# Performance work log

Hardware: AMD Instinct MI355X
Metric: run time of the kernel (lower is better)

Reference implementation:

```python
import jax, jax.numpy as jnp
import numpy as np

# config constants (match init_kwargs)
T, B = 32, 32
H, W_IN, C_IN = 128, 128, 2
FH, FW = 32, 32
CF, CP = 64, 32
OUT = 128
PATCH = 8
TOPK_R = 4
KWTA = 16
SPARSITY = 0.5
BETA = 0.9
VTH = 1.0
EVT = 0.5
PH, PW = H // PATCH, W_IN // PATCH  # 16,16


def _topk_mask(x, k):
    # mask of entries >= k-th largest along last axis
    k = min(k, x.shape[-1])
    if k <= 0:
        return jnp.zeros_like(x)
    top_vals = jax.lax.top_k(x, k)[0]
    thresh = top_vals[..., k - 1:k]
    return (x >= thresh).astype(x.dtype)


def _block_sparse_mask(w, sparsity, block=4):
    h, wk, cin, cout = w.shape
    bh, bw = h // block, wk // block
    if bh == 0 or bw == 0:
        # 3x3 kernel with block=4 degenerates to a dense (all-ones) mask
        return jnp.ones((h, wk, 1, 1), dtype=w.dtype)
    core = w[:bh * block, :bw * block, :, :]
    blocks = core.reshape(bh, block, bw, block, cin, cout)
    scores = jnp.mean(jnp.abs(blocks), axis=(1, 3, 4, 5)).reshape(-1)
    keep = max(1, int(scores.shape[0] * (1.0 - sparsity)))
    gate = _topk_mask(scores[None, :], keep).reshape(bh, bw)
    gate = jnp.repeat(jnp.repeat(gate, block, axis=0), block, axis=1)
    mask = jnp.ones((h, wk), dtype=w.dtype).at[:bh * block, :bw * block].set(gate)
    return mask[:, :, None, None]


def _conv(x, w):
    return jax.lax.conv_general_dilated(
        x, w, (1, 1), 'SAME', dimension_numbers=('NHWC', 'HWIO', 'NHWC'))


@jax.custom_vjp
def _spike(v):
    return (v > 0).astype(v.dtype)

def _spike_fwd(v):
    return _spike(v), v

def _spike_bwd(v, g):
    # superspike surrogate gradient (k=25)
    return (g / (1.0 + 25.0 * jnp.abs(v)) ** 2,)

_spike.defvjp(_spike_fwd, _spike_bwd)


def setup_inputs() -> dict:
    key = jax.random.key(0)
    ks = jax.random.split(key, 8)
    def vs_uniform(k, shape):
        # VarianceScaling(1.0, fan_avg, uniform)
        fan_in = shape[0] * shape[1] * shape[2] if len(shape) == 4 else shape[0]
        fan_out = shape[0] * shape[1] * shape[3] if len(shape) == 4 else shape[1]
        limit = float(np.sqrt(3.0 / ((fan_in + fan_out) / 2.0)))
        return jax.random.uniform(k, shape, jnp.float32, -limit, limit)
    return {
        'x_seq': jax.random.normal(ks[0], (T, B, H, W_IN, C_IN), jnp.float32),
        'w_fovea': vs_uniform(ks[1], (3, 3, C_IN, CF)),
        'w_periph': vs_uniform(ks[2], (3, 3, C_IN, CP)),
        'head_w': vs_uniform(ks[3], (CF + CP, OUT)),
        'head_b': jnp.zeros((OUT,), jnp.float32),
        'route_w': vs_uniform(ks[4], (PH * PW, OUT)),
        'route_b': jnp.zeros((OUT,), jnp.float32),
    }


def reference(x_seq, w_fovea, w_periph, head_w, head_b, route_w, route_b):
    # block-sparse masks are constant across time: apply once
    w_f = w_fovea * _block_sparse_mask(w_fovea, SPARSITY)
    w_p = w_periph * _block_sparse_mask(w_periph, SPARSITY)

    def step(carry, x_t):
        vf, vp = carry
        event_mask = (jnp.abs(x_t) > EVT).astype(x_t.dtype)
        xs = x_t * event_mask
        # region activation router: mean |x| per patch
        patches = xs.reshape(B, PH, PATCH, PW, PATCH, C_IN)
        scores = jnp.mean(jnp.abs(patches), axis=(2, 4, 5)).reshape(B, PH * PW)
        region_gate = _topk_mask(scores, TOPK_R)
        # foveal crop around the best patch
        best = jnp.argmax(scores, axis=-1)
        cy = best // PW * PATCH + PATCH // 2
        cx = best % PW * PATCH + PATCH // 2
        y0 = jnp.clip(cy - FH // 2, 0, H - FH)
        x0 = jnp.clip(cx - FW // 2, 0, W_IN - FW)
        fovea = jax.vmap(
            lambda img, y, x: jax.lax.dynamic_slice(img, (y, x, 0), (FH, FW, C_IN))
        )(xs, y0, x0)
        # fovea conv + k-WTA channel gate
        ff = _conv(fovea, w_f)
        sal = jnp.mean(jnp.abs(ff), axis=(1, 2))            # (B, CF)
        channel_gate = _topk_mask(sal, KWTA)
        ff = ff * channel_gate[:, None, None, :]
        # periphery: half-res linear resize + conv
        periph = jax.image.resize(xs, (B, H // 2, W_IN // 2, C_IN), method='linear')
        pf = _conv(periph, w_p)
        # LIF updates (beta decay, threshold, soft reset)
        vf = BETA * vf + ff
        sf = _spike(vf - VTH)
        vf = vf - sf * VTH
        vp = BETA * vp + pf
        sp = _spike(vp - VTH)
        vp = vp - sp * VTH
        fused = jnp.concatenate([jnp.mean(sf, axis=(1, 2)), jnp.mean(sp, axis=(1, 2))], axis=-1)
        logits_t = fused @ head_w + head_b + scores @ route_w + route_b
        sr_t = jnp.stack([jnp.mean(sf), jnp.mean(sp)])
        active_ratio = jnp.mean(event_mask)
        route_stats = jnp.mean(region_gate, axis=0)
        chan_stats = jnp.mean(channel_gate, axis=0)
        return (vf, vp), (logits_t, sr_t, active_ratio, route_stats, chan_stats)

    vf0 = jnp.zeros((B, FH, FW, CF), x_seq.dtype)
    vp0 = jnp.zeros((B, H // 2, W_IN // 2, CP), x_seq.dtype)
    _, (logits_seq, sr_seq, active_seq, route_seq, chan_seq) = jax.lax.scan(
        step, (vf0, vp0), x_seq)
    out = jnp.mean(logits_seq, axis=0)  # readout='mean'
    return (out, logits_seq, jnp.mean(sr_seq, axis=0), jnp.mean(active_seq),
            jnp.mean(route_seq, axis=0), jnp.mean(chan_seq, axis=0))
```

## Files before the change

kernel.cpp:

```cpp
#include <hip/hip_runtime.h>

#define T_ 32
#define B_ 32
#define H_ 128
#define W_ 128
#define C_ 2
#define NP_ 256
#define CF_ 64
#define CP_ 32
#define OUT_ 128

#define PROW 136
#define PTB  8976
#define WTB  2312

#define OFF_LOGITS 4096
#define OFF_SR     135168
#define OFF_ACTIVE 135170
#define OFF_ROUTE  135171
#define OFF_CHAN   135427

#define CNT_N 323

typedef float f2 __attribute__((ext_vector_type(2)));

__device__ __forceinline__ float f4c(const float4& v, int i) {
  switch (i & 3) { case 0: return v.x; case 1: return v.y; case 2: return v.z; default: return v.w; }
}

__global__ void __launch_bounds__(256) k_pre(const float* __restrict__ x,
    const float* __restrict__ wf,
    float* __restrict__ scores_g, float* __restrict__ P, float* __restrict__ Wfbuf,
    float* __restrict__ chan_gate, unsigned* __restrict__ cnts) {
  const int tb = blockIdx.x, tid = threadIdx.x;
  __shared__ __align__(16) float xt[34*256];
  __shared__ float sm[NP_];
  __shared__ float salred[512];
  __shared__ float salv[64];
  __shared__ unsigned wsum[4];
  __shared__ float wred[4];
  __shared__ int widx[4];
  __shared__ int2 syx;
  const float* img = x + (size_t)tb*32768;
  unsigned cnt = 0;
  for (int chunk = 0; chunk < 4; ++chunk) {
    const int r0 = chunk*16;
    __syncthreads();
    for (int i4 = tid; i4 < 34*64; i4 += 256) {
      const int rr = i4 >> 6, off4 = i4 & 63;
      const int xr = 2*r0 - 1 + rr;
      float4 vv = make_float4(0.f, 0.f, 0.f, 0.f);
      if (xr >= 0 && xr < H_) {
        vv = *reinterpret_cast<const float4*>(img + (size_t)xr*256 + off4*4);
        if (rr >= 1 && rr <= 32) {
          cnt += (fabsf(vv.x) > 0.5f) + (fabsf(vv.y) > 0.5f)
               + (fabsf(vv.z) > 0.5f) + (fabsf(vv.w) > 0.5f);
        }
        vv.x = (fabsf(vv.x) > 0.5f) ? vv.x : 0.f;
        vv.y = (fabsf(vv.y) > 0.5f) ? vv.y : 0.f;
        vv.z = (fabsf(vv.z) > 0.5f) ? vv.z : 0.f;
        vv.w = (fabsf(vv.w) > 0.5f) ? vv.w : 0.f;
      }
      *reinterpret_cast<float4*>(&xt[i4*4]) = vv;
    }
    __syncthreads();
    {
      const int patch = tid >> 2, q = tid & 3;
      const int prl = patch >> 4, pc = patch & 15;
      const int row = 1 + prl*8 + q*2;
      float s = 0.f;
#pragma unroll
      for (int r2 = 0; r2 < 2; ++r2)
#pragma unroll
        for (int j = 0; j < 4; ++j) {
          const float4 vv = *reinterpret_cast<const float4*>(&xt[(row + r2)*256 + pc*16 + j*4]);
          s += fabsf(vv.x) + fabsf(vv.y) + fabsf(vv.z) + fabsf(vv.w);
        }
      s += __shfl_down(s, 1);
      s += __shfl_down(s, 2);
      if (q == 0) {
        const float sv = s * (1.f/128.f);
        sm[chunk*64 + patch] = sv;
        scores_g[tb*NP_ + chunk*64 + patch] = sv;
      }
    }
    float* Pt = P + (size_t)tb * PTB;
    if (tid < 128) {
      const int r = tid >> 3, rem = tid & 7;
      const int px4 = rem >> 1, ci = rem & 1;
      const int px = (px4 < 2) ? (px4 - 2) : (62 + px4);
      Pt[(r0 + r + 1)*PROW + (px + 2)*2 + ci] = 0.f;
    }
    if (chunk == 0 && tid < PROW) Pt[tid] = 0.f;
    if (chunk == 3 && tid < PROW) Pt[65*PROW + tid] = 0.f;
#pragma unroll
    for (int k = 0; k < 4; ++k) {
      const int idx = k*256 + tid;
      const int col = idx & 63, row16 = idx >> 6;
      const int pr = r0 + row16;
      float wy0=0.125f, wy1=0.375f, wy2=0.375f, wy3=0.125f;
      if (pr == 0)       { wy0=0.f;     wy1=3.f/7.f; wy2=3.f/7.f; wy3=1.f/7.f; }
      else if (pr == 63) { wy0=1.f/7.f; wy1=3.f/7.f; wy2=3.f/7.f; wy3=0.f; }
      float wx0=0.125f, wx1=0.375f, wx2=0.375f, wx3=0.125f;
      if (col == 0)       { wx0=0.f;     wx1=3.f/7.f; wx2=3.f/7.f; wx3=1.f/7.f; }
      else if (col == 63) { wx0=1.f/7.f; wx1=3.f/7.f; wx2=3.f/7.f; wx3=0.f; }
      const int lr = 2*row16;
      const int cc0 = 2*col - 1;
      f2 val = (f2)0.f;
#pragma unroll
      for (int j = 0; j < 4; ++j) {
        const float wyj = (j==0)?wy0:(j==1)?wy1:(j==2)?wy2:wy3;
        f2 h = (f2)0.f;
#pragma unroll
        for (int i = 0; i < 4; ++i) {
          const float wxi = (i==0)?wx0:(i==1)?wx1:(i==2)?wx2:wx3;
          int cc = cc0 + i; cc = cc < 0 ? 0 : (cc > W_-1 ? W_-1 : cc);
          const f2 xv = *reinterpret_cast<const f2*>(&xt[(lr + j)*256 + cc*2]);
          h += wxi * xv;
        }
        val += wyj * h;
      }
      *reinterpret_cast<f2*>(&Pt[(pr + 1)*PROW + (col + 2)*2]) = val;
    }
  }
  unsigned c64 = cnt;
#pragma unroll
  for (int off = 32; off > 0; off >>= 1) c64 += __shfl_down(c64, off);
  if ((tid & 63) == 0) wsum[tid >> 6] = c64;
  __syncthreads();
  if (tid == 0) atomicAdd(&cnts[0], wsum[0] + wsum[1] + wsum[2] + wsum[3]);
  {
    const float sv_ = sm[tid];
    const int wv = tid >> 6, ln = tid & 63;
    bool masked = false;
    float v4 = 0.f;
    for (int r = 0; r < 4; ++r) {
      float cur = masked ? -1e30f : sv_;
      float m = cur;
#pragma unroll
      for (int off = 32; off > 0; off >>= 1) m = fmaxf(m, __shfl_xor(m, off));
      if (ln == 0) wred[wv] = m;
      __syncthreads();
      const float bm = fmaxf(fmaxf(wred[0], wred[1]), fmaxf(wred[2], wred[3]));
      const unsigned long long eq = __ballot(cur == bm);
      if (ln == 0) widx[wv] = eq ? (wv*64 + (int)(__ffsll((long long)eq) - 1)) : 1024;
      __syncthreads();
      const int first = min(min(widx[0], widx[1]), min(widx[2], widx[3]));
      if (tid == first) {
        masked = true;
        if (r == 0) {
          const int cy = (tid >> 4)*8 + 4, cx = (tid & 15)*8 + 4;
          int y0 = cy - 16; y0 = y0 < 0 ? 0 : (y0 > 96 ? 96 : y0);
          int x0 = cx - 16; x0 = x0 < 0 ? 0 : (x0 > 96 ? 96 : x0);
          syx = make_int2(y0, x0);
        }
      }
      if (r == 3) v4 = bm;
      __syncthreads();
    }
    if (sv_ >= v4) atomicAdd(&cnts[1 + tid], 1u);
  }
  float* tile = xt;
  for (int i = tid; i < 34*68; i += 256) tile[i] = 0.f;
  __syncthreads();
  const int2 yx = syx;
  {
    const int row = tid >> 3, seg = tid & 7;
    const float* src = img + (size_t)(yx.x + row)*256 + (yx.y + seg*4)*2;
    float4 a = *reinterpret_cast<const float4*>(src);
    float4 b4 = *reinterpret_cast<const float4*>(src + 4);
    a.x  = (fabsf(a.x)  > 0.5f) ? a.x  : 0.f;
    a.y  = (fabsf(a.y)  > 0.5f) ? a.y  : 0.f;
    a.z  = (fabsf(a.z)  > 0.5f) ? a.z  : 0.f;
    a.w  = (fabsf(a.w)  > 0.5f) ? a.w  : 0.f;
    b4.x = (fabsf(b4.x) > 0.5f) ? b4.x : 0.f;
    b4.y = (fabsf(b4.y) > 0.5f) ? b4.y : 0.f;
    b4.z = (fabsf(b4.z) > 0.5f) ? b4.z : 0.f;
    b4.w = (fabsf(b4.w) > 0.5f) ? b4.w : 0.f;
    float* dst = &tile[(row + 1)*68 + (seg*4 + 1)*2];
    *reinterpret_cast<float2*>(dst)     = make_float2(a.x, a.y);
    *reinterpret_cast<float2*>(dst + 2) = make_float2(a.z, a.w);
    *reinterpret_cast<float2*>(dst + 4) = make_float2(b4.x, b4.y);
    *reinterpret_cast<float2*>(dst + 6) = make_float2(b4.z, b4.w);
  }
  __syncthreads();
  {
    float* dst = Wfbuf + (size_t)tb*WTB;
    for (int i = tid; i < WTB/4; i += 256)
      *reinterpret_cast<float4*>(dst + i*4) = *reinterpret_cast<const float4*>(&tile[i*4]);
  }
  const int cp2 = tid & 31, xg = tid >> 5;
  const int c0 = cp2*2;
  f2 wxr[9], wyr[9];
#pragma unroll
  for (int j = 0; j < 9; ++j) {
    wxr[j] = *reinterpret_cast<const f2*>(&wf[(2*j)*CF_ + c0]);
    wyr[j] = *reinterpret_cast<const f2*>(&wf[(2*j + 1)*CF_ + c0]);
  }
  const float* tbase = &tile[xg*8];
  float4 wb[3][3];
#pragma unroll
  for (int m = 0; m < 3; ++m) {
    wb[0][m] = *reinterpret_cast<const float4*>(tbase + m*4);
    wb[1][m] = *reinterpret_cast<const float4*>(tbase + 68 + m*4);
  }
  f2 sal = (f2)0.f;
#pragma unroll
  for (int yy = 0; yy < 32; ++yy) {
#pragma unroll
    for (int m = 0; m < 3; ++m)
      wb[(yy+2)%3][m] = *reinterpret_cast<const float4*>(tbase + (yy+2)*68 + m*4);
#pragma unroll
    for (int k = 0; k < 4; ++k) {
      f2 acc = (f2)0.f;
#pragma unroll
      for (int dy = 0; dy < 3; ++dy) {
#pragma unroll
        for (int dx = 0; dx < 3; ++dx) {
          const int r = k + dx;
          const float4 f = wb[(yy+dy)%3][r >> 1];
          acc += f4c(f, (r&1)*2)     * wxr[dy*3+dx]
               + f4c(f, (r&1)*2 + 1) * wyr[dy*3+dx];
        }
      }
      sal.x += fabsf(acc.x);
      sal.y += fabsf(acc.y);
    }
  }
  salred[xg*64 + c0]     = sal.x;
  salred[xg*64 + c0 + 1] = sal.y;
  __syncthreads();
  if (tid < 64) {
    float s = 0.f;
#pragma unroll
    for (int g = 0; g < 8; ++g) s += salred[g*64 + tid];
    salv[tid] = s * (1.f/1024.f);
  }
  __syncthreads();
  if (tid < 64) {
    const float sv = salv[tid];
    int cg = 0;
    for (int q = 0; q < 64; ++q) cg += (salv[q] > sv) ? 1 : 0;
    const float gate = (cg < 16) ? 1.f : 0.f;
    chan_gate[tb*CF_ + tid] = gate;
    if (gate > 0.f) atomicAdd(&cnts[257 + tid], 1u);
  }
}

__global__ void __launch_bounds__(256, 2) k_mem(const float* __restrict__ Wfbuf,
    const float* __restrict__ P, const float* __restrict__ wf, const float* __restrict__ wp,
    const float* __restrict__ chan_gate,
    unsigned* __restrict__ fov_part, unsigned* __restrict__ per_part) {
  __shared__ __align__(16) float lds[2*1360];
  const int tid = threadIdx.x;
  const int w = tid >> 6, l = tid & 63;
  int zp;
  asm volatile("v_mov_b32 %0, 0" : "=v"(zp));
  if (blockIdx.x < 1024) {
    const int blk = blockIdx.x;
    const int b = blk >> 5, rem = blk & 31, cp = rem >> 1, half = rem & 1;
    const int ch0 = cp*4;
    const int brow = w*4 + (l >> 4);
    const int po = (l & 15)*4;
    f2 w01[18], w23[18];
#pragma unroll
    for (int k = 0; k < 18; ++k) {
      w01[k] = *reinterpret_cast<const f2*>(&wf[k*CF_ + ch0 + zp]);
      w23[k] = *reinterpret_cast<const f2*>(&wf[k*CF_ + ch0 + zp + 2]);
    }
    const float* gsrc = Wfbuf + (size_t)b*WTB + half*16*68;
    const float* gp = chan_gate + b*CF_ + ch0 + zp;
    const unsigned ob01 = (unsigned)((b*32 + cp*2)*8 + half*4 + w);
    f2 va01 = (f2)0.f, vb01 = (f2)0.f, va23 = (f2)0.f, vb23 = (f2)0.f;
    float4 r0, r1;
    r0 = *reinterpret_cast<const float4*>(gsrc + tid*4);
    if (tid < 50) r1 = *reinterpret_cast<const float4*>(gsrc + (tid + 256)*4);
    *reinterpret_cast<float4*>(&lds[tid*4]) = r0;
    if (tid < 50) *reinterpret_cast<float4*>(&lds[(tid + 256)*4]) = r1;
    int cur = 0;
    for (int t = 0; t < T_; ++t) {
      __syncthreads();
      if (t + 1 < T_) {
        const float* gn = gsrc + (size_t)(t + 1)*(B_*WTB);
        r0 = *reinterpret_cast<const float4*>(gn + tid*4);
        if (tid < 50) r1 = *reinterpret_cast<const float4*>(gn + (tid + 256)*4);
      }
      __builtin_amdgcn_sched_barrier(0);
      const f2 g01 = *reinterpret_cast<const f2*>(gp + (size_t)t*B_*CF_);
      const f2 g23 = *reinterpret_cast<const f2*>(gp + (size_t)t*B_*CF_ + 2);
      const float* Lb = &lds[cur*1360];
      f2 aa01 = (f2)0.f, ab01 = (f2)0.f, aa23 = (f2)0.f, ab23 = (f2)0.f;
#pragma unroll
      for (int dy = 0; dy < 3; ++dy) {
        const float4 fa = *reinterpret_cast<const float4*>(Lb + (brow + dy)*68 + po);
        const float4 fb = *reinterpret_cast<const float4*>(Lb + (brow + dy)*68 + po + 4);
        {
          const f2 w0 = w01[dy*6], w0y = w01[dy*6+1], w1 = w01[dy*6+2],
                   w1y = w01[dy*6+3], w2 = w01[dy*6+4], w2y = w01[dy*6+5];
          aa01 += fa.x*w0 + fa.y*w0y + fa.z*w1 + fa.w*w1y + fb.x*w2 + fb.y*w2y;
          ab01 += fa.z*w0 + fa.w*w0y + fb.x*w1 + fb.y*w1y + fb.z*w2 + fb.w*w2y;
        }
        {
          const f2 w0 = w23[dy*6], w0y = w23[dy*6+1], w1 = w23[dy*6+2],
                   w1y = w23[dy*6+3], w2 = w23[dy*6+4], w2y = w23[dy*6+5];
          aa23 += fa.x*w0 + fa.y*w0y + fa.z*w1 + fa.w*w1y + fb.x*w2 + fb.y*w2y;
          ab23 += fa.z*w0 + fa.w*w0y + fb.x*w1 + fb.y*w1y + fb.z*w2 + fb.w*w2y;
        }
      }
      f2 na01 = 0.9f*va01 + aa01*g01;
      f2 nb01 = 0.9f*vb01 + ab01*g01;
      f2 na23 = 0.9f*va23 + aa23*g23;
      f2 nb23 = 0.9f*vb23 + ab23*g23;
      const bool s0a = na01.x > 1.f, s1a = na01.y > 1.f, s0b = nb01.x > 1.f, s1b = nb01.y > 1.f;
      const bool s2a = na23.x > 1.f, s3a = na23.y > 1.f, s2b = nb23.x > 1.f, s3b = nb23.y > 1.f;
      va01.x = s0a ? na01.x - 1.f : na01.x;  va01.y = s1a ? na01.y - 1.f : na01.y;
      vb01.x = s0b ? nb01.x - 1.f : nb01.x;  vb01.y = s1b ? nb01.y - 1.f : nb01.y;
      va23.x = s2a ? na23.x - 1.f : na23.x;  va23.y = s3a ? na23.y - 1.f : na23.y;
      vb23.x = s2b ? nb23.x - 1.f : nb23.x;  vb23.y = s3b ? nb23.y - 1.f : nb23.y;
      const unsigned p01 =
          (unsigned)(__popcll(__ballot(s0a)) + __popcll(__ballot(s0b)))
        | ((unsigned)(__popcll(__ballot(s1a)) + __popcll(__ballot(s1b))) << 16);
      const unsigned p23 =
          (unsigned)(__popcll(__ballot(s2a)) + __popcll(__ballot(s2b)))
        | ((unsigned)(__popcll(__ballot(s3a)) + __popcll(__ballot(s3b))) << 16);
      if (l == 0) {
        fov_part[ob01 + (unsigned)t*8192u]     = p01;
        fov_part[ob01 + 8 + (unsigned)t*8192u] = p23;
      }
      if (t + 1 < T_) {
        float* Lw = &lds[(cur ^ 1)*1360];
        *reinterpret_cast<float4*>(Lw + tid*4) = r0;
        if (tid < 50) *reinterpret_cast<float4*>(Lw + (tid + 256)*4) = r1;
      }
      cur ^= 1;
    }
  } else {
    const int blk = blockIdx.x - 1024;
    const int b = blk >> 6, rem = blk & 63, cp = rem >> 3, rq = rem & 7;
    const int ch0 = cp*4;
    const int brow = w*2 + (l >> 5);
    const int po = (l & 31)*4;
    f2 w01[18], w23[18];
#pragma unroll
    for (int k = 0; k < 18; ++k) {
      w01[k] = *reinterpret_cast<const f2*>(&wp[k*CP_ + ch0 + zp]);
      w23[k] = *reinterpret_cast<const f2*>(&wp[k*CP_ + ch0 + zp + 2]);
    }
    const float* gsrc = P + (size_t)b*PTB + rq*8*PROW;
    const unsigned ob01 = (unsigned)((b*16 + cp*2)*32 + rq*4 + w);
    f2 va01 = (f2)0.f, vb01 = (f2)0.f, va23 = (f2)0.f, vb23 = (f2)0.f;
    float4 r0, r1;
    r0 = *reinterpret_cast<const float4*>(gsrc + tid*4);
    if (tid < 84) r1 = *reinterpret_cast<const float4*>(gsrc + (tid + 256)*4);
    *reinterpret_cast<float4*>(&lds[tid*4]) = r0;
    if (tid < 84) *reinterpret_cast<float4*>(&lds[(tid + 256)*4]) = r1;
    int cur = 0;
    for (int t = 0; t < T_; ++t) {
      __syncthreads();
      if (t + 1 < T_) {
        const float* gn = gsrc + (size_t)(t + 1)*(B_*PTB);
        r0 = *reinterpret_cast<const float4*>(gn + tid*4);
        if (tid < 84) r1 = *reinterpret_cast<const float4*>(gn + (tid + 256)*4);
      }
      __builtin_amdgcn_sched_barrier(0);
      const float* Lb = &lds[cur*1360];
      f2 aa01 = (f2)0.f, ab01 = (f2)0.f, aa23 = (f2)0.f, ab23 = (f2)0.f;
#pragma unroll
      for (int dy = 0; dy < 3; ++dy) {
        const float4 f0 = *reinterpret_cast<const float4*>(Lb + (brow + dy)*136 + po);
        const float4 f1 = *reinterpret_cast<const float4*>(Lb + (brow + dy)*136 + po + 4);
        const float4 f2v = *reinterpret_cast<const float4*>(Lb + (brow + dy)*136 + po + 8);
        {
          const f2 w0 = w01[dy*6], w0y = w01[dy*6+1], w1 = w01[dy*6+2],
                   w1y = w01[dy*6+3], w2 = w01[dy*6+4], w2y = w01[dy*6+5];
          aa01 += f0.z*w0 + f0.w*w0y + f1.x*w1 + f1.y*w1y + f1.z*w2 + f1.w*w2y;
          ab01 += f1.x*w0 + f1.y*w0y + f1.z*w1 + f1.w*w1y + f2v.x*w2 + f2v.y*w2y;
        }
        {
          const f2 w0 = w23[dy*6], w0y = w23[dy*6+1], w1 = w23[dy*6+2],
                   w1y = w23[dy*6+3], w2 = w23[dy*6+4], w2y = w23[dy*6+5];
          aa23 += f0.z*w0 + f0.w*w0y + f1.x*w1 + f1.y*w1y + f1.z*w2 + f1.w*w2y;
          ab23 += f1.x*w0 + f1.y*w0y + f1.z*w1 + f1.w*w1y + f2v.x*w2 + f2v.y*w2y;
        }
      }
      f2 na01 = 0.9f*va01 + aa01;
      f2 nb01 = 0.9f*vb01 + ab01;
      f2 na23 = 0.9f*va23 + aa23;
      f2 nb23 = 0.9f*vb23 + ab23;
      const bool s0a = na01.x > 1.f, s1a = na01.y > 1.f, s0b = nb01.x > 1.f, s1b = nb01.y > 1.f;
      const bool s2a = na23.x > 1.f, s3a = na23.y > 1.f, s2b = nb23.x > 1.f, s3b = nb23.y > 1.f;
      va01.x = s0a ? na01.x - 1.f : na01.x;  va01.y = s1a ? na01.y - 1.f : na01.y;
      vb01.x = s0b ? nb01.x - 1.f : nb01.x;  vb01.y = s1b ? nb01.y - 1.f : nb01.y;
      va23.x = s2a ? na23.x - 1.f : na23.x;  va23.y = s3a ? na23.y - 1.f : na23.y;
      vb23.x = s2b ? nb23.x - 1.f : nb23.x;  vb23.y = s3b ? nb23.y - 1.f : nb23.y;
      const unsigned p01 =
          (unsigned)(__popcll(__ballot(s0a)) + __popcll(__ballot(s0b)))
        | ((unsigned)(__popcll(__ballot(s1a)) + __popcll(__ballot(s1b))) << 16);
      const unsigned p23 =
          (unsigned)(__popcll(__ballot(s2a)) + __popcll(__ballot(s2b)))
        | ((unsigned)(__popcll(__ballot(s3a)) + __popcll(__ballot(s3b))) << 16);
      if (l == 0) {
        per_part[ob01 + (unsigned)t*16384u]      = p01;
        per_part[ob01 + 32 + (unsigned)t*16384u] = p23;
      }
      if (t + 1 < T_) {
        float* Lw = &lds[(cur ^ 1)*1360];
        *reinterpret_cast<float4*>(Lw + tid*4) = r0;
        if (tid < 84) *reinterpret_cast<float4*>(Lw + (tid + 256)*4) = r1;
      }
      cur ^= 1;
    }
  }
}

__global__ void __launch_bounds__(256) k_logits(const float* __restrict__ scores,
    const unsigned* __restrict__ fov_part, const unsigned* __restrict__ per_part,
    const float* __restrict__ head_w, const float* __restrict__ head_b,
    const float* __restrict__ route_w, const float* __restrict__ route_b,
    float* __restrict__ logits, unsigned* __restrict__ tot) {
  const int tb = blockIdx.x, tid = threadIdx.x;
  __shared__ float sc[NP_];
  __shared__ float fu[96];
  sc[tid] = scores[tb*NP_ + tid];
  if (tid < 64) {
    const unsigned* fp = fov_part + (size_t)tb*256;
    const int cp = tid >> 1, sh = (tid & 1)*16;
    unsigned fsum = 0;
#pragma unroll
    for (int i = 0; i < 8; ++i) fsum += (fp[cp*8 + i] >> sh) & 0xFFFFu;
    fu[tid] = (float)fsum * (1.f/1024.f);
    unsigned r = fsum;
#pragma unroll
    for (int off = 32; off > 0; off >>= 1) r += __shfl_down(r, off);
    if (tid == 0) atomicAdd(&tot[0], r);
  } else if (tid < 128) {
    const int c = tid - 64;
    unsigned psum = 0;
    if (c < 32) {
      const unsigned* pp = per_part + (size_t)tb*512;
      const int cp = c >> 1, sh = (c & 1)*16;
#pragma unroll 8
      for (int i = 0; i < 32; ++i) psum += (pp[cp*32 + i] >> sh) & 0xFFFFu;
      fu[64 + c] = (float)psum * (1.f/4096.f);
    }
    unsigned r = psum;
#pragma unroll
    for (int off = 32; off > 0; off >>= 1) r += __shfl_down(r, off);
    if (tid == 64) atomicAdd(&tot[1], r);
  }
  __syncthreads();
  if (tid < 128) {
    const int o = tid;
    float acc = head_b[o] + route_b[o];
#pragma unroll 8
    for (int k = 0; k < 96; ++k)  acc += fu[k]*head_w[k*OUT_ + o];
#pragma unroll 8
    for (int p = 0; p < NP_; ++p) acc += sc[p]*route_w[p*OUT_ + o];
    logits[tb*OUT_ + o] = acc;
  }
}

__global__ void __launch_bounds__(256) k_final(const float* __restrict__ logits,
    float* __restrict__ dout, const unsigned* __restrict__ cnts) {
  const int blk = blockIdx.x, tid = threadIdx.x;
  if (blk < 16) {
    const int idx = blk*256 + tid;
    const int b = idx >> 7, o = idx & 127;
    float s = 0.f;
#pragma unroll
    for (int t = 0; t < T_; ++t) s += logits[(t*B_ + b)*OUT_ + o];
    dout[idx] = s * (1.f/32.f);
  } else {
    if (tid == 0) {
      dout[OFF_SR]     = (float)cnts[321] * (1.f/67108864.f);
      dout[OFF_SR + 1] = (float)cnts[322] * (1.f/134217728.f);
      dout[OFF_ACTIVE] = (float)cnts[0]   * (1.f/33554432.f);
    }
    dout[OFF_ROUTE + tid] = (float)cnts[1 + tid] * (1.f/1024.f);
    if (tid < 64) dout[OFF_CHAN + tid] = (float)cnts[257 + tid] * (1.f/1024.f);
  }
}

extern "C" void kernel_launch(void* const* d_in, const int* in_sizes, int n_in,
                              void* d_out, int out_size, void* d_ws, size_t ws_size,
                              hipStream_t stream) {
  const float* x       = (const float*)d_in[0];
  const float* wf      = (const float*)d_in[1];
  const float* wp      = (const float*)d_in[2];
  const float* head_w  = (const float*)d_in[3];
  const float* head_b  = (const float*)d_in[4];
  const float* route_w = (const float*)d_in[5];
  const float* route_b = (const float*)d_in[6];
  float* out = (float*)d_out;

  float*    ws_P      = (float*)d_ws;
  float*    ws_Wf     = ws_P + (size_t)1024*PTB;
  float*    ws_scores = ws_Wf + (size_t)1024*WTB;
  float*    ws_gate   = ws_scores + T_*B_*NP_;
  unsigned* fov_part  = (unsigned*)(ws_gate + T_*B_*CF_);
  unsigned* per_part  = fov_part + (size_t)T_*B_*256;
  unsigned* ws_cnt    = per_part + (size_t)T_*B_*512;

  hipMemsetAsync(ws_cnt, 0, CNT_N*sizeof(unsigned), stream);

  k_pre   <<<T_*B_, 256, 0, stream>>>(x, wf, ws_scores, ws_P, ws_Wf, ws_gate, ws_cnt);
  k_mem   <<<3072,  256, 0, stream>>>(ws_Wf, ws_P, wf, wp, ws_gate, fov_part, per_part);
  k_logits<<<T_*B_, 256, 0, stream>>>(ws_scores, fov_part, per_part, head_w, head_b,
                                      route_w, route_b, out + OFF_LOGITS, ws_cnt + 321);
  k_final <<<17, 256, 0, stream>>>(out + OFF_LOGITS, out, ws_cnt);
}
```

Before: 238.8 us.

## Register-block periphery LIF conv to four outputs per thread with taller tiles

The periphery branch of k_mem now has each thread compute four adjacent output pixels instead of two. Each block covers 16 input rows instead of 8, so the number of periphery blocks halves and the relative halo overhead per tile shrinks. Each LDS row segment is loaded once and reused across neighbouring outputs. Spike-count partials are repacked to the new layout, and k_logits and the workspace offsets are adjusted to match. In exchange it doubles the LDS buffer, adds more accumulator registers, and leaves fewer blocks to spread across the GPU.

```diff
diff --git a/kernel.cpp b/kernel.cpp
--- a/kernel.cpp
+++ b/kernel.cpp
@@ -251,7 +251,7 @@
     const float* __restrict__ P, const float* __restrict__ wf, const float* __restrict__ wp,
     const float* __restrict__ chan_gate,
     unsigned* __restrict__ fov_part, unsigned* __restrict__ per_part) {
-  __shared__ __align__(16) float lds[2*1360];
+  __shared__ __align__(16) float lds[2*2448];
   const int tid = threadIdx.x;
   const int w = tid >> 6, l = tid & 63;
   int zp;
@@ -288,7 +288,7 @@
       __builtin_amdgcn_sched_barrier(0);
       const f2 g01 = *reinterpret_cast<const f2*>(gp + (size_t)t*B_*CF_);
       const f2 g23 = *reinterpret_cast<const f2*>(gp + (size_t)t*B_*CF_ + 2);
-      const float* Lb = &lds[cur*1360];
+      const float* Lb = &lds[cur*2448];
       f2 aa01 = (f2)0.f, ab01 = (f2)0.f, aa23 = (f2)0.f, ab23 = (f2)0.f;
 #pragma unroll
       for (int dy = 0; dy < 3; ++dy) {
@@ -328,7 +328,7 @@
         fov_part[ob01 + 8 + (unsigned)t*8192u] = p23;
       }
       if (t + 1 < T_) {
-        float* Lw = &lds[(cur ^ 1)*1360];
+        float* Lw = &lds[(cur ^ 1)*2448];
         *reinterpret_cast<float4*>(Lw + tid*4) = r0;
         if (tid < 50) *reinterpret_cast<float4*>(Lw + (tid + 256)*4) = r1;
       }
@@ -336,77 +336,83 @@
     }
   } else {
     const int blk = blockIdx.x - 1024;
-    const int b = blk >> 6, rem = blk & 63, cp = rem >> 3, rq = rem & 7;
+    const int b = blk >> 5, rem = blk & 31, cp = rem >> 2, rq = rem & 3;
     const int ch0 = cp*4;
-    const int brow = w*2 + (l >> 5);
-    const int po = (l & 31)*4;
+    const int srow = w*4 + (l >> 4);
+    const int po = (l & 15)*8;
     f2 w01[18], w23[18];
 #pragma unroll
     for (int k = 0; k < 18; ++k) {
       w01[k] = *reinterpret_cast<const f2*>(&wp[k*CP_ + ch0 + zp]);
       w23[k] = *reinterpret_cast<const f2*>(&wp[k*CP_ + ch0 + zp + 2]);
     }
-    const float* gsrc = P + (size_t)b*PTB + rq*8*PROW;
-    const unsigned ob01 = (unsigned)((b*16 + cp*2)*32 + rq*4 + w);
-    f2 va01 = (f2)0.f, vb01 = (f2)0.f, va23 = (f2)0.f, vb23 = (f2)0.f;
-    float4 r0, r1;
+    const float* gsrc = P + (size_t)b*PTB + rq*16*PROW;
+    const unsigned ob = (unsigned)((b*16 + cp*2)*16 + rq*4 + w);
+    f2 va01[4], va23[4];
+#pragma unroll
+    for (int k = 0; k < 4; ++k) { va01[k] = (f2)0.f; va23[k] = (f2)0.f; }
+    float4 r0, r1, r2;
     r0 = *reinterpret_cast<const float4*>(gsrc + tid*4);
-    if (tid < 84) r1 = *reinterpret_cast<const float4*>(gsrc + (tid + 256)*4);
+    r1 = *reinterpret_cast<const float4*>(gsrc + (tid + 256)*4);
+    if (tid < 100) r2 = *reinterpret_cast<const float4*>(gsrc + (tid + 512)*4);
     *reinterpret_cast<float4*>(&lds[tid*4]) = r0;
-    if (tid < 84) *reinterpret_cast<float4*>(&lds[(tid + 256)*4]) = r1;
+    *reinterpret_cast<float4*>(&lds[(tid + 256)*4]) = r1;
+    if (tid < 100) *reinterpret_cast<float4*>(&lds[(tid + 512)*4]) = r2;
     int cur = 0;
     for (int t = 0; t < T_; ++t) {
       __syncthreads();
       if (t + 1 < T_) {
         const float* gn = gsrc + (size_t)(t + 1)*(B_*PTB);
         r0 = *reinterpret_cast<const float4*>(gn + tid*4);
-        if (tid < 84) r1 = *reinterpret_cast<const float4*>(gn + (tid + 256)*4);
+        r1 = *reinterpret_cast<const float4*>(gn + (tid + 256)*4);
+        if (tid < 100) r2 = *reinterpret_cast<const float4*>(gn + (tid + 512)*4);
       }
       __builtin_amdgcn_sched_barrier(0);
-      const float* Lb = &lds[cur*1360];
-      f2 aa01 = (f2)0.f, ab01 = (f2)0.f, aa23 = (f2)0.f, ab23 = (f2)0.f;
+      const float* Lb = &lds[cur*2448];
+      f2 a01[4], a23[4];
+#pragma unroll
+      for (int k = 0; k < 4; ++k) { a01[k] = (f2)0.f; a23[k] = (f2)0.f; }
 #pragma unroll
       for (int dy = 0; dy < 3; ++dy) {
-        const float4 f0 = *reinterpret_cast<const float4*>(Lb + (brow + dy)*136 + po);
-        const float4 f1 = *reinterpret_cast<const float4*>(Lb + (brow + dy)*136 + po + 4);
-        const float4 f2v = *reinterpret_cast<const float4*>(Lb + (brow + dy)*136 + po + 8);
-        {
-          const f2 w0 = w01[dy*6], w0y = w01[dy*6+1], w1 = w01[dy*6+2],
-                   w1y = w01[dy*6+3], w2 = w01[dy*6+4], w2y = w01[dy*6+5];
-          aa01 += f0.z*w0 + f0.w*w0y + f1.x*w1 + f1.y*w1y + f1.z*w2 + f1.w*w2y;
-          ab01 += f1.x*w0 + f1.y*w0y + f1.z*w1 + f1.w*w1y + f2v.x*w2 + f2v.y*w2y;
-        }
-        {
-          const f2 w0 = w23[dy*6], w0y = w23[dy*6+1], w1 = w23[dy*6+2],
-                   w1y = w23[dy*6+3], w2 = w23[dy*6+4], w2y = w23[dy*6+5];
-          aa23 += f0.z*w0 + f0.w*w0y + f1.x*w1 + f1.y*w1y + f1.z*w2 + f1.w*w2y;
-          ab23 += f1.x*w0 + f1.y*w0y + f1.z*w1 + f1.w*w1y + f2v.x*w2 + f2v.y*w2y;
-        }
-      }
-      f2 na01 = 0.9f*va01 + aa01;
-      f2 nb01 = 0.9f*vb01 + ab01;
-      f2 na23 = 0.9f*va23 + aa23;
-      f2 nb23 = 0.9f*vb23 + ab23;
-      const bool s0a = na01.x > 1.f, s1a = na01.y > 1.f, s0b = nb01.x > 1.f, s1b = nb01.y > 1.f;
-      const bool s2a = na23.x > 1.f, s3a = na23.y > 1.f, s2b = nb23.x > 1.f, s3b = nb23.y > 1.f;
-      va01.x = s0a ? na01.x - 1.f : na01.x;  va01.y = s1a ? na01.y - 1.f : na01.y;
-      vb01.x = s0b ? nb01.x - 1.f : nb01.x;  vb01.y = s1b ? nb01.y - 1.f : nb01.y;
-      va23.x = s2a ? na23.x - 1.f : na23.x;  va23.y = s3a ? na23.y - 1.f : na23.y;
-      vb23.x = s2b ? nb23.x - 1.f : nb23.x;  vb23.y = s3b ? nb23.y - 1.f : nb23.y;
-      const unsigned p01 =
-          (unsigned)(__popcll(__ballot(s0a)) + __popcll(__ballot(s0b)))
-        | ((unsigned)(__popcll(__ballot(s1a)) + __popcll(__ballot(s1b))) << 16);
-      const unsigned p23 =
-          (unsigned)(__popcll(__ballot(s2a)) + __popcll(__ballot(s2b)))
-        | ((unsigned)(__popcll(__ballot(s3a)) + __popcll(__ballot(s3b))) << 16);
+        float4 F[4];
+#pragma unroll
+        for (int m = 0; m < 4; ++m)
+          F[m] = *reinterpret_cast<const float4*>(Lb + (srow + dy)*136 + po + m*4);
+#pragma unroll
+        for (int k = 0; k < 4; ++k)
+#pragma unroll
+          for (int dx = 0; dx < 3; ++dx) {
+            const int e = 2*(k + dx + 1);
+            const float cx = f4c(F[e >> 2], e & 3);
+            const float cy = f4c(F[(e + 1) >> 2], (e + 1) & 3);
+            a01[k] += cx*w01[dy*6 + dx*2] + cy*w01[dy*6 + dx*2 + 1];
+            a23[k] += cx*w23[dy*6 + dx*2] + cy*w23[dy*6 + dx*2 + 1];
+          }
+      }
+      unsigned c0 = 0, c1 = 0, c2 = 0, c3 = 0;
+#pragma unroll
+      for (int k = 0; k < 4; ++k) {
+        f2 n01 = 0.9f*va01[k] + a01[k];
+        f2 n23 = 0.9f*va23[k] + a23[k];
+        const bool b0 = n01.x > 1.f, b1 = n01.y > 1.f, b2 = n23.x > 1.f, b3 = n23.y > 1.f;
+        va01[k].x = b0 ? n01.x - 1.f : n01.x;
+        va01[k].y = b1 ? n01.y - 1.f : n01.y;
+        va23[k].x = b2 ? n23.x - 1.f : n23.x;
+        va23[k].y = b3 ? n23.y - 1.f : n23.y;
+        c0 += (unsigned)__popcll(__ballot(b0));
+        c1 += (unsigned)__popcll(__ballot(b1));
+        c2 += (unsigned)__popcll(__ballot(b2));
+        c3 += (unsigned)__popcll(__ballot(b3));
+      }
       if (l == 0) {
-        per_part[ob01 + (unsigned)t*16384u]      = p01;
-        per_part[ob01 + 32 + (unsigned)t*16384u] = p23;
+        per_part[ob + (unsigned)t*8192u]      = c0 | (c1 << 16);
+        per_part[ob + 16 + (unsigned)t*8192u] = c2 | (c3 << 16);
       }
       if (t + 1 < T_) {
-        float* Lw = &lds[(cur ^ 1)*1360];
+        float* Lw = &lds[(cur ^ 1)*2448];
         *reinterpret_cast<float4*>(Lw + tid*4) = r0;
-        if (tid < 84) *reinterpret_cast<float4*>(Lw + (tid + 256)*4) = r1;
+        *reinterpret_cast<float4*>(Lw + (tid + 256)*4) = r1;
+        if (tid < 100) *reinterpret_cast<float4*>(Lw + (tid + 512)*4) = r2;
       }
       cur ^= 1;
     }
@@ -437,10 +443,10 @@
     const int c = tid - 64;
     unsigned psum = 0;
     if (c < 32) {
-      const unsigned* pp = per_part + (size_t)tb*512;
+      const unsigned* pp = per_part + (size_t)tb*256;
       const int cp = c >> 1, sh = (c & 1)*16;
 #pragma unroll 8
-      for (int i = 0; i < 32; ++i) psum += (pp[cp*32 + i] >> sh) & 0xFFFFu;
+      for (int i = 0; i < 16; ++i) psum += (pp[cp*16 + i] >> sh) & 0xFFFFu;
       fu[64 + c] = (float)psum * (1.f/4096.f);
     }
     unsigned r = psum;
@@ -499,12 +505,12 @@
   float*    ws_gate   = ws_scores + T_*B_*NP_;
   unsigned* fov_part  = (unsigned*)(ws_gate + T_*B_*CF_);
   unsigned* per_part  = fov_part + (size_t)T_*B_*256;
-  unsigned* ws_cnt    = per_part + (size_t)T_*B_*512;
+  unsigned* ws_cnt    = per_part + (size_t)T_*B_*256;
 
   hipMemsetAsync(ws_cnt, 0, CNT_N*sizeof(unsigned), stream);
 
   k_pre   <<<T_*B_, 256, 0, stream>>>(x, wf, ws_scores, ws_P, ws_Wf, ws_gate, ws_cnt);
-  k_mem   <<<3072,  256, 0, stream>>>(ws_Wf, ws_P, wf, wp, ws_gate, fov_part, per_part);
+  k_mem   <<<2048,  256, 0, stream>>>(ws_Wf, ws_P, wf, wp, ws_gate, fov_part, per_part);
   k_logits<<<T_*B_, 256, 0, stream>>>(ws_scores, fov_part, per_part, head_w, head_b,
                                       route_w, route_b, out + OFF_LOGITS, ws_cnt + 321);
   k_final <<<17, 256, 0, stream>>>(out + OFF_LOGITS, out, ws_cnt);
```

Result: slower. 253.1 us (+6.0%).
